# Kernel optimization log

Measured on AMD Instinct MI355X. Metric: run time of the kernel, lower is better.

The kernel has to match this reference:

```python
import jax, jax.numpy as jnp
import numpy as np

EPS = 1e-5
IOU_SCALE = 10000.0
NEG_TH_ACGT = 3000.0   # int(10000*0.3)
POS_TH_ACGT = 5000.0   # int(10000*0.5)
NUM_POS_RPN = 128
NUM_NEG_RPN = 128

B, N_AC, N_GT = 8, 128 * 128 * 9, 64


def _make_boxes(u):
    # u in [0,1): (yc, xc, sh, sw) -> valid YXYX boxes
    yc, xc = u[..., 0], u[..., 1]
    hh = 0.05 + 0.25 * u[..., 2]
    ww = 0.05 + 0.25 * u[..., 3]
    return jnp.stack([yc - 0.5 * hh, xc - 0.5 * ww, yc + 0.5 * hh, xc + 0.5 * ww], axis=-1)


def setup_inputs() -> dict:
    key = jax.random.key(0)
    k1, k2, k3 = jax.random.split(key, 3)
    anchors = _make_boxes(jax.random.uniform(k1, (N_AC, 4)))
    gt_boxes = _make_boxes(jax.random.uniform(k2, (B, N_GT, 4)))
    deltas = 0.1 * jax.random.normal(k3, (B, N_AC, 4), dtype=jnp.float32)
    return {"anchors": anchors, "gt_boxes": gt_boxes, "deltas": deltas}


def _area(b):
    return jnp.maximum(b[..., 2] - b[..., 0], 0.0) * jnp.maximum(b[..., 3] - b[..., 1], 0.0)


def _iou(ac, gt):
    # ac: (A,4), gt: (B,G,4) -> scaled IoU (B,A,G)
    a = ac[None, :, None, :]
    g = gt[:, None, :, :]
    yi = jnp.maximum(a[..., 0], g[..., 0])
    xi = jnp.maximum(a[..., 1], g[..., 1])
    ya = jnp.minimum(a[..., 2], g[..., 2])
    xa = jnp.minimum(a[..., 3], g[..., 3])
    inter = jnp.maximum(ya - yi, 0.0) * jnp.maximum(xa - xi, 0.0)
    union = _area(a) + _area(g) - inter
    return IOU_SCALE * inter / (union + EPS)


def _bbox2delta(bl, br):
    wr, hr = br[..., 3] - br[..., 1], br[..., 2] - br[..., 0]
    xcr, ycr = br[..., 1] + 0.5 * wr, br[..., 0] + 0.5 * hr
    wr_c, hr_c = jnp.maximum(wr, EPS), jnp.maximum(hr, EPS)
    wl, hl = bl[..., 3] - bl[..., 1], bl[..., 2] - bl[..., 0]
    xcl, ycl = bl[..., 1] + 0.5 * wl, bl[..., 0] + 0.5 * hl
    d = jnp.stack([(xcl - xcr) / wr_c, (ycl - ycr) / hr_c,
                   jnp.log(wl / wr_c), jnp.log(hl / hr_c)], axis=-1)
    return jnp.clip(d, -10.0, 10.0)


def _delta2bbox(base, diff):
    wb, hb = base[..., 3] - base[..., 1], base[..., 2] - base[..., 0]
    xc = base[..., 1] + 0.5 * wb + wb * diff[..., 0]
    yc = base[..., 0] + 0.5 * hb + hb * diff[..., 1]
    w_ = wb * jnp.exp(diff[..., 2])
    h_ = hb * jnp.exp(diff[..., 3])
    # from_xywh -> YXYX
    return jnp.stack([yc - 0.5 * h_, xc - 0.5 * w_, yc + 0.5 * h_, xc + 0.5 * w_], axis=-1)


def _sample_mask(mask, num, key):
    th = num / (jnp.sum(mask, axis=-1, keepdims=True) + 1e-6)
    rand = jax.random.uniform(key, mask.shape, dtype=jnp.float32)
    return jnp.where(rand < th, 1.0, 0.0) * mask


def reference(anchors, gt_boxes, deltas):
    ious = _iou(anchors, gt_boxes)                 # (B, A, G)
    best_iou = jnp.max(ious, axis=-1)              # (B, A)
    best_idx = jnp.argmax(ious, axis=-1)           # (B, A)
    gt_best = jnp.take_along_axis(
        gt_boxes, jnp.broadcast_to(best_idx[:, :, None], best_idx.shape + (4,)), axis=1)

    pos = best_iou > POS_TH_ACGT
    neg = best_iou < NEG_TH_ACGT
    # fg: matched GT box; bkg: all -2; ignore: all -1
    bx_tgt = jnp.where(pos[..., None], gt_best,
                       jnp.where(neg[..., None], -2.0, -1.0))

    coor_sum = jnp.sum(bx_tgt, axis=-1)
    kp, kn = jax.random.split(jax.random.key(42))
    mask_pos = _sample_mask(jnp.where(coor_sum > -4.0, 1.0, 0.0), NUM_POS_RPN, kp)
    mask_neg = _sample_mask(jnp.where(coor_sum <= -8.0, 1.0, 0.0), NUM_NEG_RPN, kn)

    ac_b = jnp.broadcast_to(anchors[None], bx_tgt.shape)
    # safe left operand so log() stays finite for non-positive anchors
    bx_tgt_safe = jnp.where(pos[..., None], bx_tgt, ac_b)
    del_tgt = _bbox2delta(bx_tgt_safe, ac_b) * mask_pos[..., None]   # (B, A, 4)

    proposals = _delta2bbox(anchors[None], deltas)                    # (B, A, 4)
    return jnp.concatenate([proposals, del_tgt], axis=-1)            # (B, A, 8)
```

## Files before the change

kernel.cpp:

```cpp
#include <hip/hip_runtime.h>
#include <hip/hip_cooperative_groups.h>
#include <stdint.h>

namespace cg = cooperative_groups;

#define NAC 147456
#define NGT 64
#define NB  8
#define APT 3
#define BLK 256
#define GX  (NAC / (BLK * APT))

__host__ __device__ static inline uint32_t tf_rotl(uint32_t x, uint32_t d) {
  return (x << d) | (x >> (32u - d));
}

__host__ __device__ static inline void threefry2x32(
    uint32_t k0, uint32_t k1, uint32_t x0, uint32_t x1,
    uint32_t* o0, uint32_t* o1)
{
  const uint32_t ks2 = k0 ^ k1 ^ 0x1BD11BDAu;
  x0 += k0; x1 += k1;
#define TFR(r) { x0 += x1; x1 = tf_rotl(x1, (r)); x1 ^= x0; }
  TFR(13u) TFR(15u) TFR(26u) TFR(6u)   x0 += k1;  x1 += ks2 + 1u;
  TFR(17u) TFR(29u) TFR(16u) TFR(24u)  x0 += ks2; x1 += k0 + 2u;
  TFR(13u) TFR(15u) TFR(26u) TFR(6u)   x0 += k0;  x1 += k1 + 3u;
  TFR(17u) TFR(29u) TFR(16u) TFR(24u)  x0 += k1;  x1 += ks2 + 4u;
  TFR(13u) TFR(15u) TFR(26u) TFR(6u)   x0 += ks2; x1 += k0 + 5u;
#undef TFR
  *o0 = x0; *o1 = x1;
}

__device__ static inline float4 bbox2delta_calc(const float4& a, const float4& g)
{
  const float wr  = a.w - a.y,          hr  = a.z - a.x;
  const float xcr = a.y + 0.5f * wr,    ycr = a.x + 0.5f * hr;
  const float wrc = fmaxf(wr, 1e-5f),   hrc = fmaxf(hr, 1e-5f);
  const float wl  = g.w - g.y,          hl  = g.z - g.x;
  const float xcl = g.y + 0.5f * wl,    ycl = g.x + 0.5f * hl;
  float4 r;
  r.x = fminf(fmaxf((xcl - xcr) / wrc, -10.0f), 10.0f);
  r.y = fminf(fmaxf((ycl - ycr) / hrc, -10.0f), 10.0f);
  r.z = fminf(fmaxf(__logf(wl / wrc),  -10.0f), 10.0f);
  r.w = fminf(fmaxf(__logf(hl / hrc),  -10.0f), 10.0f);
  return r;
}

__global__ __launch_bounds__(BLK) void k_fused(
    const float* __restrict__ anchors,
    const float* __restrict__ gt,
    const float* __restrict__ deltas,
    float* __restrict__ out,
    int* __restrict__ counts,
    uint32_t kp0, uint32_t kp1)
{
  __shared__ __align__(16) float4 gbox[NGT];
  __shared__ __align__(16) float  garea[NGT];
  __shared__ __align__(16) float  gae[NGT];
  __shared__ int s_cnt;
  const int b   = blockIdx.y;
  const int tid = threadIdx.x;

  if (tid == 0) s_cnt = 0;
  if (tid < NGT) {
    float4 g = reinterpret_cast<const float4*>(gt)[b * NGT + tid];
    const float ga = fmaxf(g.z - g.x, 0.0f) * fmaxf(g.w - g.y, 0.0f);
    gbox[tid]  = g;
    garea[tid] = ga;
    gae[tid]   = ga + 1e-5f;
  }
  __syncthreads();

  const int base = blockIdx.x * (BLK * APT) + tid;

  float4 a[APT];
  float  areaA[APT], num[APT], Tb[APT];
  int    bidx[APT];
#pragma unroll
  for (int t = 0; t < APT; ++t) {
    a[t] = reinterpret_cast<const float4*>(anchors)[base + t * BLK];
    areaA[t] = fmaxf(a[t].z - a[t].x, 0.0f) * fmaxf(a[t].w - a[t].y, 0.0f);
    num[t]  = 0.0f;
    Tb[t]   = 1.0f;
    bidx[t] = 0;
  }

  for (int jj = 0; jj < NGT; jj += 4) {
    const float4 te4 = *reinterpret_cast<const float4*>(&gae[jj]);
    const float4 g0 = gbox[jj + 0];
    const float4 g1 = gbox[jj + 1];
    const float4 g2 = gbox[jj + 2];
    const float4 g3 = gbox[jj + 3];
    const float4 gs[4] = { g0, g1, g2, g3 };
#pragma unroll
    for (int u = 0; u < 4; ++u) {
      const float4 g  = gs[u];
      const float  te = (&te4.x)[u];
      const int    j  = jj + u;
#pragma unroll
      for (int t = 0; t < APT; ++t) {
        float yi = fmaxf(a[t].x, g.x);
        float xi = fmaxf(a[t].y, g.y);
        float ya = fminf(a[t].z, g.z);
        float xa = fminf(a[t].w, g.w);
        float inter = fmaxf(ya - yi, 0.0f) * fmaxf(xa - xi, 0.0f);
        float Tj = areaA[t] + te;
        bool upd = inter * Tb[t] > num[t] * Tj;
        num[t]  = upd ? inter : num[t];
        Tb[t]   = upd ? Tj    : Tb[t];
        bidx[t] = upd ? j     : bidx[t];
      }
    }
  }

  int posm = 0;
  int npos = 0;
#pragma unroll
  for (int t = 0; t < APT; ++t) {
    const int i = base + t * BLK;
    const float gaB = garea[bidx[t]];
    const float den = ((areaA[t] + gaB) - num[t]) + 1e-5f;
    const float best_iou = (10000.0f * num[t]) / den;
    const bool pos = best_iou > 5000.0f;
    posm |= (pos ? 1 : 0) << t;

    const float4 d = reinterpret_cast<const float4*>(deltas)[b * NAC + i];
    const float wb = a[t].w - a[t].y, hb = a[t].z - a[t].x;
    const float xc = a[t].y + 0.5f * wb + wb * d.x;
    const float yc = a[t].x + 0.5f * hb + hb * d.y;
    const float w_ = wb * __expf(d.z);
    const float h_ = hb * __expf(d.w);

    float* rowp = out + ((size_t)b * NAC + i) * 8;
    reinterpret_cast<float4*>(rowp)[0] =
        make_float4(yc - 0.5f * h_, xc - 0.5f * w_, yc + 0.5f * h_, xc + 0.5f * w_);

    unsigned long long m = __ballot(pos);
    if ((tid & 63) == 0) npos += (int)__popcll(m);
  }
  if ((tid & 63) == 0 && npos)
    atomicAdd(&s_cnt, npos);
  __syncthreads();
  if (tid == 0 && s_cnt)
    atomicAdd(&counts[b], s_cnt);

  cg::this_grid().sync();

  const int tot = __hip_atomic_load(&counts[b], __ATOMIC_RELAXED,
                                    __HIP_MEMORY_SCOPE_AGENT);
  const float th = 128.0f / ((float)tot + 1e-6f);

#pragma unroll
  for (int t = 0; t < APT; ++t) {
    const int i = base + t * BLK;
    const int f = b * NAC + i;
    float4 r = make_float4(0.f, 0.f, 0.f, 0.f);
    if ((posm >> t) & 1) {
      uint32_t o0, o1;
      threefry2x32(kp0, kp1, 0u, (uint32_t)f, &o0, &o1);
      const uint32_t bits = o0 ^ o1;
      union { uint32_t u; float flt; } cv;
      cv.u = (bits >> 9) | 0x3F800000u;
      if (cv.flt - 1.0f < th) {
        const float4 g = gbox[bidx[t]];
        r = bbox2delta_calc(a[t], g);
      }
    }
    reinterpret_cast<float4*>(out + (size_t)f * 8)[1] = r;
  }
}

__global__ __launch_bounds__(BLK) void k1_classify(
    const float* __restrict__ anchors,
    const float* __restrict__ gt,
    const float* __restrict__ deltas,
    float* __restrict__ out,
    int* __restrict__ counts)
{
  __shared__ __align__(16) float4 gbox[NGT];
  __shared__ __align__(16) float  garea[NGT];
  __shared__ __align__(16) float  gae[NGT];
  __shared__ int s_cnt;
  const int b   = blockIdx.y;
  const int tid = threadIdx.x;

  if (tid == 0) s_cnt = 0;
  if (tid < NGT) {
    float4 g = reinterpret_cast<const float4*>(gt)[b * NGT + tid];
    const float ga = fmaxf(g.z - g.x, 0.0f) * fmaxf(g.w - g.y, 0.0f);
    gbox[tid]  = g;
    garea[tid] = ga;
    gae[tid]   = ga + 1e-5f;
  }
  __syncthreads();

  const int base = blockIdx.x * (BLK * APT) + tid;

  float4 a[APT];
  float  areaA[APT], num[APT], Tb[APT];
  int    bidx[APT];
#pragma unroll
  for (int t = 0; t < APT; ++t) {
    a[t] = reinterpret_cast<const float4*>(anchors)[base + t * BLK];
    areaA[t] = fmaxf(a[t].z - a[t].x, 0.0f) * fmaxf(a[t].w - a[t].y, 0.0f);
    num[t]  = 0.0f;
    Tb[t]   = 1.0f;
    bidx[t] = 0;
  }

  for (int jj = 0; jj < NGT; jj += 4) {
    const float4 te4 = *reinterpret_cast<const float4*>(&gae[jj]);
    const float4 g0 = gbox[jj + 0];
    const float4 g1 = gbox[jj + 1];
    const float4 g2 = gbox[jj + 2];
    const float4 g3 = gbox[jj + 3];
    const float4 gs[4] = { g0, g1, g2, g3 };
#pragma unroll
    for (int u = 0; u < 4; ++u) {
      const float4 g  = gs[u];
      const float  te = (&te4.x)[u];
      const int    j  = jj + u;
#pragma unroll
      for (int t = 0; t < APT; ++t) {
        float yi = fmaxf(a[t].x, g.x);
        float xi = fmaxf(a[t].y, g.y);
        float ya = fminf(a[t].z, g.z);
        float xa = fminf(a[t].w, g.w);
        float inter = fmaxf(ya - yi, 0.0f) * fmaxf(xa - xi, 0.0f);
        float Tj = areaA[t] + te;
        bool upd = inter * Tb[t] > num[t] * Tj;
        num[t]  = upd ? inter : num[t];
        Tb[t]   = upd ? Tj    : Tb[t];
        bidx[t] = upd ? j     : bidx[t];
      }
    }
  }

  int npos = 0;
#pragma unroll
  for (int t = 0; t < APT; ++t) {
    const int i = base + t * BLK;
    const float gaB = garea[bidx[t]];
    const float den = ((areaA[t] + gaB) - num[t]) + 1e-5f;
    const float best_iou = (10000.0f * num[t]) / den;
    const bool pos = best_iou > 5000.0f;

    const float4 d = reinterpret_cast<const float4*>(deltas)[b * NAC + i];
    const float wb = a[t].w - a[t].y, hb = a[t].z - a[t].x;
    const float xc = a[t].y + 0.5f * wb + wb * d.x;
    const float yc = a[t].x + 0.5f * hb + hb * d.y;
    const float w_ = wb * __expf(d.z);
    const float h_ = hb * __expf(d.w);

    float* rowp = out + ((size_t)b * NAC + i) * 8;
    reinterpret_cast<float4*>(rowp)[0] =
        make_float4(yc - 0.5f * h_, xc - 0.5f * w_, yc + 0.5f * h_, xc + 0.5f * w_);
    reinterpret_cast<float4*>(rowp)[1] =
        make_float4(pos ? (float)(bidx[t] + 1) : 0.0f, 0.f, 0.f, 0.f);

    unsigned long long m = __ballot(pos);
    if ((tid & 63) == 0) npos += (int)__popcll(m);
  }
  if ((tid & 63) == 0 && npos)
    atomicAdd(&s_cnt, npos);
  __syncthreads();

  if (tid == 0 && s_cnt) atomicAdd(&counts[b], s_cnt);
}

__global__ __launch_bounds__(256) void k2_fallback(
    const float* __restrict__ anchors,
    const float* __restrict__ gt,
    float* __restrict__ out,
    const int* __restrict__ counts,
    uint32_t kp0, uint32_t kp1)
{
  const int b = blockIdx.y;
  const int i = blockIdx.x * 256 + threadIdx.x;
  const int f = b * NAC + i;
  float* rowp = out + (size_t)f * 8;

  const float flag = rowp[4];
  if (flag == 0.0f) return;

  const float th = 128.0f / ((float)counts[b] + 1e-6f);

  uint32_t o0, o1;
  threefry2x32(kp0, kp1, 0u, (uint32_t)f, &o0, &o1);
  const uint32_t bits = o0 ^ o1;
  union { uint32_t u; float flt; } cv;
  cv.u = (bits >> 9) | 0x3F800000u;

  if (cv.flt - 1.0f < th) {
    const float4 a = reinterpret_cast<const float4*>(anchors)[i];
    const float4 g = reinterpret_cast<const float4*>(gt)[b * NGT + ((int)flag - 1)];
    float4 r = bbox2delta_calc(a, g);
    *reinterpret_cast<float4*>(rowp + 4) = r;
  } else {
    reinterpret_cast<float4*>(rowp)[1] = make_float4(0.f, 0.f, 0.f, 0.f);
  }
}

extern "C" void kernel_launch(void* const* d_in, const int* in_sizes, int n_in,
                              void* d_out, int out_size, void* d_ws, size_t ws_size,
                              hipStream_t stream)
{
  const float* anchors = (const float*)d_in[0];
  const float* gt      = (const float*)d_in[1];
  const float* deltas  = (const float*)d_in[2];
  float* out   = (float*)d_out;
  int* counts  = (int*)d_ws;

  uint32_t kp0, kp1;
  threefry2x32(0u, 42u, 0u, 0u, &kp0, &kp1);

  static int coop_ok = -1;
  if (coop_ok < 0) {
    int dev = 0, c = 0;
    hipGetDevice(&dev);
    hipDeviceGetAttribute(&c, hipDeviceAttributeCooperativeLaunch, dev);
    coop_ok = c;
  }

  hipMemsetAsync(counts, 0, NB * sizeof(int), stream);

  bool launched = false;
  if (coop_ok) {
    void* params[] = { (void*)&anchors, (void*)&gt, (void*)&deltas,
                       (void*)&out, (void*)&counts, (void*)&kp0, (void*)&kp1 };
    hipError_t e = hipLaunchCooperativeKernel(
        reinterpret_cast<void*>(k_fused), dim3(GX, NB), dim3(BLK),
        params, 0, stream);
    launched = (e == hipSuccess);
    if (!launched) coop_ok = 0;
  }
  if (!launched) {
    dim3 g1(GX, NB);
    k1_classify<<<g1, dim3(BLK), 0, stream>>>(anchors, gt, deltas, out, counts);
    dim3 g2(NAC / 256, NB);
    k2_fallback<<<g2, dim3(256), 0, stream>>>(anchors, gt, out, counts,
                                              kp0, kp1);
  }
}
```

Measured before the change: 119.6 us.

## Replace cooperative grid sync with per-batch arrival counter barrier

Drops the cooperative launch and grid-wide sync. Each batch row now waits on its own atomic arrival counter with a sleep-spin loop and reads the positive count once per block through shared memory. The kernel also gains a launch_bounds occupancy hint and drops one fmax clamp in the IoU loop, since a negative width only lowers the product and cannot win the max. The cost removed is the cooperative-launch overhead and the full-grid barrier. The risk is a deadlock if not all blocks are co-resident, because a normal launch gives no residency guarantee.

```diff
diff --git a/kernel.cpp b/kernel.cpp
--- a/kernel.cpp
+++ b/kernel.cpp
@@ -1,8 +1,5 @@
 #include <hip/hip_runtime.h>
-#include <hip/hip_cooperative_groups.h>
 #include <stdint.h>
-
-namespace cg = cooperative_groups;
 
 #define NAC 147456
 #define NGT 64
@@ -46,18 +43,20 @@
   return r;
 }
 
-__global__ __launch_bounds__(BLK) void k_fused(
+__global__ __launch_bounds__(BLK, 6) void k_fused(
     const float* __restrict__ anchors,
     const float* __restrict__ gt,
     const float* __restrict__ deltas,
     float* __restrict__ out,
-    int* __restrict__ counts,
+    int* __restrict__ cnt,
+    int* __restrict__ arr,
     uint32_t kp0, uint32_t kp1)
 {
   __shared__ __align__(16) float4 gbox[NGT];
   __shared__ __align__(16) float  garea[NGT];
   __shared__ __align__(16) float  gae[NGT];
   __shared__ int s_cnt;
+  __shared__ int s_tot;
   const int b   = blockIdx.y;
   const int tid = threadIdx.x;
 
@@ -85,33 +84,38 @@
     bidx[t] = 0;
   }
 
+#define IOU_ONE(gv, te, jv)                                              \
+  {                                                                      \
+    const float4 g_ = (gv);                                              \
+    const float  te_ = (te);                                             \
+    const int    j_  = (jv);                                             \
+    _Pragma("unroll")                                                    \
+    for (int t = 0; t < APT; ++t) {                                      \
+      float yi = fmaxf(a[t].x, g_.x);                                    \
+      float xi = fmaxf(a[t].y, g_.y);                                    \
+      float ya = fminf(a[t].z, g_.z);                                    \
+      float xa = fminf(a[t].w, g_.w);                                    \
+      float inter = fmaxf(ya - yi, 0.0f) * (xa - xi);                    \
+      float Tj = areaA[t] + te_;                                         \
+      bool upd = inter * Tb[t] > num[t] * Tj;                            \
+      num[t]  = upd ? inter : num[t];                                    \
+      Tb[t]   = upd ? Tj    : Tb[t];                                     \
+      bidx[t] = upd ? j_    : bidx[t];                                   \
+    }                                                                    \
+  }
+
   for (int jj = 0; jj < NGT; jj += 4) {
     const float4 te4 = *reinterpret_cast<const float4*>(&gae[jj]);
     const float4 g0 = gbox[jj + 0];
     const float4 g1 = gbox[jj + 1];
     const float4 g2 = gbox[jj + 2];
     const float4 g3 = gbox[jj + 3];
-    const float4 gs[4] = { g0, g1, g2, g3 };
-#pragma unroll
-    for (int u = 0; u < 4; ++u) {
-      const float4 g  = gs[u];
-      const float  te = (&te4.x)[u];
-      const int    j  = jj + u;
-#pragma unroll
-      for (int t = 0; t < APT; ++t) {
-        float yi = fmaxf(a[t].x, g.x);
-        float xi = fmaxf(a[t].y, g.y);
-        float ya = fminf(a[t].z, g.z);
-        float xa = fminf(a[t].w, g.w);
-        float inter = fmaxf(ya - yi, 0.0f) * fmaxf(xa - xi, 0.0f);
-        float Tj = areaA[t] + te;
-        bool upd = inter * Tb[t] > num[t] * Tj;
-        num[t]  = upd ? inter : num[t];
-        Tb[t]   = upd ? Tj    : Tb[t];
-        bidx[t] = upd ? j     : bidx[t];
-      }
-    }
-  }
+    IOU_ONE(g0, te4.x, jj + 0)
+    IOU_ONE(g1, te4.y, jj + 1)
+    IOU_ONE(g2, te4.z, jj + 2)
+    IOU_ONE(g3, te4.w, jj + 3)
+  }
+#undef IOU_ONE
 
   int posm = 0;
   int npos = 0;
@@ -141,14 +145,23 @@
   if ((tid & 63) == 0 && npos)
     atomicAdd(&s_cnt, npos);
   __syncthreads();
-  if (tid == 0 && s_cnt)
-    atomicAdd(&counts[b], s_cnt);
-
-  cg::this_grid().sync();
-
-  const int tot = __hip_atomic_load(&counts[b], __ATOMIC_RELAXED,
-                                    __HIP_MEMORY_SCOPE_AGENT);
-  const float th = 128.0f / ((float)tot + 1e-6f);
+
+  if (tid == 0) {
+    if (s_cnt)
+      __hip_atomic_fetch_add(&cnt[b], s_cnt, __ATOMIC_RELAXED,
+                             __HIP_MEMORY_SCOPE_AGENT);
+    __hip_atomic_fetch_add(&arr[b], 1, __ATOMIC_RELEASE,
+                           __HIP_MEMORY_SCOPE_AGENT);
+    while (__hip_atomic_load(&arr[b], __ATOMIC_ACQUIRE,
+                             __HIP_MEMORY_SCOPE_AGENT) < GX) {
+      __builtin_amdgcn_s_sleep(2);
+    }
+    s_tot = __hip_atomic_load(&cnt[b], __ATOMIC_RELAXED,
+                              __HIP_MEMORY_SCOPE_AGENT);
+  }
+  __syncthreads();
+
+  const float th = 128.0f / ((float)s_tot + 1e-6f);
 
 #pragma unroll
   for (int t = 0; t < APT; ++t) {
@@ -162,8 +175,7 @@
       union { uint32_t u; float flt; } cv;
       cv.u = (bits >> 9) | 0x3F800000u;
       if (cv.flt - 1.0f < th) {
-        const float4 g = gbox[bidx[t]];
-        r = bbox2delta_calc(a[t], g);
+        r = bbox2delta_calc(a[t], gbox[bidx[t]]);
       }
     }
     reinterpret_cast<float4*>(out + (size_t)f * 8)[1] = r;
@@ -226,7 +238,7 @@
         float xi = fmaxf(a[t].y, g.y);
         float ya = fminf(a[t].z, g.z);
         float xa = fminf(a[t].w, g.w);
-        float inter = fmaxf(ya - yi, 0.0f) * fmaxf(xa - xi, 0.0f);
+        float inter = fmaxf(ya - yi, 0.0f) * (xa - xi);
         float Tj = areaA[t] + te;
         bool upd = inter * Tb[t] > num[t] * Tj;
         num[t]  = upd ? inter : num[t];
@@ -308,37 +320,24 @@
   const float* anchors = (const float*)d_in[0];
   const float* gt      = (const float*)d_in[1];
   const float* deltas  = (const float*)d_in[2];
-  float* out   = (float*)d_out;
-  int* counts  = (int*)d_ws;
+  float* out  = (float*)d_out;
+  int* cnt = (int*)d_ws;
+  int* arr = (int*)d_ws + NB;
 
   uint32_t kp0, kp1;
   threefry2x32(0u, 42u, 0u, 0u, &kp0, &kp1);
 
-  static int coop_ok = -1;
-  if (coop_ok < 0) {
-    int dev = 0, c = 0;
-    hipGetDevice(&dev);
-    hipDeviceGetAttribute(&c, hipDeviceAttributeCooperativeLaunch, dev);
-    coop_ok = c;
-  }
-
-  hipMemsetAsync(counts, 0, NB * sizeof(int), stream);
-
-  bool launched = false;
-  if (coop_ok) {
-    void* params[] = { (void*)&anchors, (void*)&gt, (void*)&deltas,
-                       (void*)&out, (void*)&counts, (void*)&kp0, (void*)&kp1 };
-    hipError_t e = hipLaunchCooperativeKernel(
-        reinterpret_cast<void*>(k_fused), dim3(GX, NB), dim3(BLK),
-        params, 0, stream);
-    launched = (e == hipSuccess);
-    if (!launched) coop_ok = 0;
-  }
-  if (!launched) {
+  hipMemsetAsync(d_ws, 0, 2 * NB * sizeof(int), stream);
+
+  if (ws_size >= 2 * NB * sizeof(int)) {
     dim3 g1(GX, NB);
-    k1_classify<<<g1, dim3(BLK), 0, stream>>>(anchors, gt, deltas, out, counts);
+    k_fused<<<g1, dim3(BLK), 0, stream>>>(anchors, gt, deltas, out,
+                                          cnt, arr, kp0, kp1);
+  } else {
+    dim3 g1(GX, NB);
+    k1_classify<<<g1, dim3(BLK), 0, stream>>>(anchors, gt, deltas, out, cnt);
     dim3 g2(NAC / 256, NB);
-    k2_fallback<<<g2, dim3(256), 0, stream>>>(anchors, gt, out, counts,
+    k2_fallback<<<g2, dim3(256), 0, stream>>>(anchors, gt, out, cnt,
                                               kp0, kp1);
   }
 }
```

Measured after the change: 330.1 us. +176.0%, slower.
